# Optimization experiments

Measured on AMD Instinct MI355X. Metric: run time of the kernel, lower is better.

Reference implementation:

```python
import jax, jax.numpy as jnp
import numpy as np

START_IX = 62
END_IX = 63
NEG = -10000.0

def setup_inputs() -> dict:
    key = jax.random.key(0)
    k1, k2 = jax.random.split(key)
    B, S, T = 512, 1024, 64
    feats = jax.random.normal(k1, (B, S, T), dtype=jnp.float32)
    transitions = jax.random.normal(k2, (T, T), dtype=jnp.float32)
    # CRF constraints: nothing transitions into START; nothing transitions out of END
    transitions = transitions.at[START_IX, :].set(NEG).at[:, END_IX].set(NEG)
    return {"feats": feats, "transitions": transitions}

def reference(feats, transitions):
    # Viterbi decode (module forward). feats: [B,S,T], transitions: [T,T] (next, prev)
    B, S, T = feats.shape
    init = jnp.full((B, T), NEG, dtype=feats.dtype).at[:, START_IX].set(0.0)

    def step(fv, feat):  # fv [B,T], feat [B,T]
        # next_tag_var[b, next, prev] = fv[b, prev] + transitions[next, prev]
        nv = fv[:, None, :] + transitions[None, :, :]
        bp = jnp.argmax(nv, axis=2)                     # [B,T] best previous tag
        fv_new = jnp.max(nv, axis=2) + feat             # [B,T]
        return fv_new, bp

    fv, bptrs = jax.lax.scan(step, init, jnp.transpose(feats, (1, 0, 2)))  # bptrs [S,B,T]
    terminal = fv + transitions[END_IX][None, :]
    path_score = jnp.max(terminal, axis=1)              # [B]
    best_tag = jnp.argmax(terminal, axis=1)             # [B]

    def back(tag, bp):  # tag [B], bp [B,T]
        prev = jnp.take_along_axis(bp, tag[:, None], axis=1)[:, 0]
        return prev, tag

    _, tags_rev = jax.lax.scan(back, best_tag, bptrs[::-1])  # [S,B]: tags S-1..0
    best_path = jnp.transpose(tags_rev[::-1])                # [B,S]
    return path_score, best_path
```

## Files before the change

kernel.cpp:

```cpp
#include <hip/hip_runtime.h>

#define NEGV (-10000.0f)

constexpr int Bb = 512;
constexpr int Ss = 1024;
constexpr int Tt = 64;

typedef __attribute__((address_space(1))) const unsigned int guint_t;
typedef __attribute__((address_space(3))) unsigned int luint_t;

__global__ __launch_bounds__(256, 2) void viterbi_fused(
    const float* __restrict__ feats,
    const float* __restrict__ trans,
    float* __restrict__ path_score,
    float* __restrict__ best_path)
{
    __shared__ float ftile[2][8][Tt];
    __shared__ uint2 partials[2][4][Tt];
    __shared__ float fvb[4][16];
    __shared__ unsigned char bp_lds[Ss][Tt];
    __shared__ unsigned char ccomp[32][Tt];
    __shared__ int btags[32];

    const int b    = blockIdx.x;
    const int tid  = threadIdx.x;
    const int wid  = tid >> 6;
    const int lane = tid & 63;

    const float* fb = feats + (size_t)b * (Ss * Tt);

    const float* tr = trans + lane * Tt + (wid << 4);
    float4 t0 = *(const float4*)(tr + 0);
    float4 t1 = *(const float4*)(tr + 4);
    float4 t2 = *(const float4*)(tr + 8);
    float4 t3 = *(const float4*)(tr + 12);
    float tend = trans[63 * Tt + lane];

    if (wid == 0) {
#pragma unroll
        for (int i = 0; i < 2; ++i)
            __builtin_amdgcn_global_load_lds(
                (guint_t*)(fb + i * 256 + lane * 4),
                (luint_t*)((unsigned int*)&ftile[0][0][0] + i * 256),
                16, 0, 0);
        asm volatile("s_waitcnt vmcnt(0)" ::: "memory");
    }
    __syncthreads();

    float fv  = (lane == 62) ? 0.0f : NEGV;
    int  comp = lane;

    for (int t = 0; t < 128; ++t) {
        if (wid == 0 && t + 1 < 128) {
            const float* src = fb + (size_t)(t + 1) * 512;
            unsigned int* dst = (unsigned int*)&ftile[(t + 1) & 1][0][0];
#pragma unroll
            for (int i = 0; i < 2; ++i)
                __builtin_amdgcn_global_load_lds(
                    (guint_t*)(src + i * 256 + lane * 4),
                    (luint_t*)(dst + i * 256),
                    16, 0, 0);
        }
#pragma unroll
        for (int i = 0; i < 8; ++i) {
            const int s = t * 8 + i;
            float featv = ftile[t & 1][i][lane];

            if ((lane >> 4) == wid) fvb[wid][lane & 15] = fv;
            float4 q0 = *(float4*)&fvb[wid][0];
            float4 q1 = *(float4*)&fvb[wid][4];
            float4 q2 = *(float4*)&fvb[wid][8];
            float4 q3 = *(float4*)&fvb[wid][12];

            float mq0, mq1, mq2, mq3; int xq0, xq1, xq2, xq3;
#define QUAD(K, QV, TV, MQ, XQ) { \
            float ca = QV.x + TV.x, cb = QV.y + TV.y, cc = QV.z + TV.z, cd = QV.w + TV.w; \
            float mm = ca; int xx = 4*K + 0; \
            if (cb > mm) { mm = cb; xx = 4*K + 1; } \
            if (cc > mm) { mm = cc; xx = 4*K + 2; } \
            if (cd > mm) { mm = cd; xx = 4*K + 3; } \
            MQ = mm; XQ = xx; }
            QUAD(0, q0, t0, mq0, xq0)
            QUAD(1, q1, t1, mq1, xq1)
            QUAD(2, q2, t2, mq2, xq2)
            QUAD(3, q3, t3, mq3, xq3)
#undef QUAD
            float mp = mq0; int xp = xq0;
            if (mq1 > mp) { mp = mq1; xp = xq1; }
            if (mq2 > mp) { mp = mq2; xp = xq2; }
            if (mq3 > mp) { mp = mq3; xp = xq3; }
            int gix = (wid << 4) + xp;

            partials[i & 1][wid][lane] = make_uint2(__float_as_uint(mp), (unsigned)gix);

            if (i == 7) {
                asm volatile("" : "+v"(featv));
                if (wid == 0) asm volatile("s_waitcnt vmcnt(0)" ::: "memory");
            }
            __syncthreads();

            uint2 r0 = partials[i & 1][0][lane];
            uint2 r1 = partials[i & 1][1][lane];
            uint2 r2 = partials[i & 1][2][lane];
            uint2 r3 = partials[i & 1][3][lane];
            float mb = __uint_as_float(r0.x); int ib = (int)r0.y;
            float mw;
            mw = __uint_as_float(r1.x); if (mw > mb) { mb = mw; ib = (int)r1.y; }
            mw = __uint_as_float(r2.x); if (mw > mb) { mb = mw; ib = (int)r2.y; }
            mw = __uint_as_float(r3.x); if (mw > mb) { mb = mw; ib = (int)r3.y; }

            if (wid == 0) {
                bp_lds[s][lane] = (unsigned char)ib;
                comp = __shfl(comp, ib);
                if ((s & 31) == 31) { ccomp[s >> 5][lane] = (unsigned char)comp; comp = lane; }
            }
            fv = mb + featv;
        }
    }

    if (wid == 0) {
        float mr = fv + tend; int ir = lane;
#pragma unroll
        for (int off = 32; off >= 1; off >>= 1) {
            float mo = __shfl_xor(mr, off);
            int   io = __shfl_xor(ir, off);
            bool take = (mo > mr) || ((mo == mr) && (io < ir));
            mr = take ? mo : mr; ir = take ? io : ir;
        }
        if (lane == 0) {
            path_score[b] = mr;
            int tag = ir;
            for (int c = 31; c >= 0; --c) {
                btags[c] = tag;
                tag = ccomp[c][tag];
            }
        }
    }
    __syncthreads();

    if (wid == 0 && lane < 32) {
        int tag = btags[lane];
        float* op = best_path + (size_t)b * Ss + lane * 32;
        for (int i = 31; i >= 0; --i) {
            op[i] = (float)tag;
            tag = bp_lds[lane * 32 + i][tag];
        }
    }
}

extern "C" void kernel_launch(void* const* d_in, const int* in_sizes, int n_in,
                              void* d_out, int out_size, void* d_ws, size_t ws_size,
                              hipStream_t stream) {
    const float* feats = (const float*)d_in[0];
    const float* trans = (const float*)d_in[1];

    float* path_score = (float*)d_out;
    float* best_path  = (float*)d_out + Bb;

    viterbi_fused<<<Bb, 256, 0, stream>>>(feats, trans, path_score, best_path);
}
```

Before: 591.1 us.

## Broadcast fv via readlane and defer argmax byte resolution off the critical path

Replaces the LDS round-trip that broadcasts fv within each wave with v_readlane instructions, and moves argmax tracking out of the serial max chain. Only the max value is exchanged across waves before the barrier. Each wave then recovers its local index by equality match and writes one byte into a packed word. Wave 0 resolves the backpointer one step late, and the prefetch moves to wave 3 to lighten wave 0. This shortens the per-step critical path between barriers, at the cost of extra compare work, a deferred final step, and tie-breaking that now depends on exact float equality.

```diff
diff --git a/kernel.cpp b/kernel.cpp
--- a/kernel.cpp
+++ b/kernel.cpp
@@ -16,8 +16,8 @@
     float* __restrict__ best_path)
 {
     __shared__ float ftile[2][8][Tt];
-    __shared__ uint2 partials[2][4][Tt];
-    __shared__ float fvb[4][16];
+    __shared__ float vpart[2][4][Tt];
+    __shared__ unsigned int ipart[2][Tt];
     __shared__ unsigned char bp_lds[Ss][Tt];
     __shared__ unsigned char ccomp[32][Tt];
     __shared__ int btags[32];
@@ -26,17 +26,22 @@
     const int tid  = threadIdx.x;
     const int wid  = tid >> 6;
     const int lane = tid & 63;
+    const int base = wid << 4;
 
     const float* fb = feats + (size_t)b * (Ss * Tt);
 
-    const float* tr = trans + lane * Tt + (wid << 4);
-    float4 t0 = *(const float4*)(tr + 0);
-    float4 t1 = *(const float4*)(tr + 4);
-    float4 t2 = *(const float4*)(tr + 8);
-    float4 t3 = *(const float4*)(tr + 12);
+    float trow[16];
+    {
+        const float* tr = trans + lane * Tt + base;
+        float4* tv = (float4*)trow;
+        tv[0] = *(const float4*)(tr + 0);
+        tv[1] = *(const float4*)(tr + 4);
+        tv[2] = *(const float4*)(tr + 8);
+        tv[3] = *(const float4*)(tr + 12);
+    }
     float tend = trans[63 * Tt + lane];
 
-    if (wid == 0) {
+    if (wid == 3) {
 #pragma unroll
         for (int i = 0; i < 2; ++i)
             __builtin_amdgcn_global_load_lds(
@@ -51,7 +56,7 @@
     int  comp = lane;
 
     for (int t = 0; t < 128; ++t) {
-        if (wid == 0 && t + 1 < 128) {
+        if (wid == 3 && t + 1 < 128) {
             const float* src = fb + (size_t)(t + 1) * 512;
             unsigned int* dst = (unsigned int*)&ftile[(t + 1) & 1][0][0];
 #pragma unroll
@@ -64,61 +69,71 @@
 #pragma unroll
         for (int i = 0; i < 8; ++i) {
             const int s = t * 8 + i;
+            const int p = s & 1;
             float featv = ftile[t & 1][i][lane];
 
-            if ((lane >> 4) == wid) fvb[wid][lane & 15] = fv;
-            float4 q0 = *(float4*)&fvb[wid][0];
-            float4 q1 = *(float4*)&fvb[wid][4];
-            float4 q2 = *(float4*)&fvb[wid][8];
-            float4 q3 = *(float4*)&fvb[wid][12];
+            float c[16];
+#pragma unroll
+            for (int j = 0; j < 16; ++j) {
+                float g = __int_as_float(
+                    __builtin_amdgcn_readlane(__float_as_int(fv), base + j));
+                c[j] = g + trow[j];
+            }
+            float a0 = fmaxf(fmaxf(c[0],  c[1]),  c[2]);
+            float a1 = fmaxf(fmaxf(c[3],  c[4]),  c[5]);
+            float a2 = fmaxf(fmaxf(c[6],  c[7]),  c[8]);
+            float a3 = fmaxf(fmaxf(c[9],  c[10]), c[11]);
+            float a4 = fmaxf(fmaxf(c[12], c[13]), c[14]);
+            float m  = fmaxf(fmaxf(fmaxf(a0, a1), fmaxf(a2, a3)), fmaxf(a4, c[15]));
 
-            float mq0, mq1, mq2, mq3; int xq0, xq1, xq2, xq3;
-#define QUAD(K, QV, TV, MQ, XQ) { \
-            float ca = QV.x + TV.x, cb = QV.y + TV.y, cc = QV.z + TV.z, cd = QV.w + TV.w; \
-            float mm = ca; int xx = 4*K + 0; \
-            if (cb > mm) { mm = cb; xx = 4*K + 1; } \
-            if (cc > mm) { mm = cc; xx = 4*K + 2; } \
-            if (cd > mm) { mm = cd; xx = 4*K + 3; } \
-            MQ = mm; XQ = xx; }
-            QUAD(0, q0, t0, mq0, xq0)
-            QUAD(1, q1, t1, mq1, xq1)
-            QUAD(2, q2, t2, mq2, xq2)
-            QUAD(3, q3, t3, mq3, xq3)
-#undef QUAD
-            float mp = mq0; int xp = xq0;
-            if (mq1 > mp) { mp = mq1; xp = xq1; }
-            if (mq2 > mp) { mp = mq2; xp = xq2; }
-            if (mq3 > mp) { mp = mq3; xp = xq3; }
-            int gix = (wid << 4) + xp;
-
-            partials[i & 1][wid][lane] = make_uint2(__float_as_uint(mp), (unsigned)gix);
+            vpart[p][wid][lane] = m;
 
             if (i == 7) {
                 asm volatile("" : "+v"(featv));
-                if (wid == 0) asm volatile("s_waitcnt vmcnt(0)" ::: "memory");
+                if (wid == 3) asm volatile("s_waitcnt vmcnt(0)" ::: "memory");
             }
             __syncthreads();
 
-            uint2 r0 = partials[i & 1][0][lane];
-            uint2 r1 = partials[i & 1][1][lane];
-            uint2 r2 = partials[i & 1][2][lane];
-            uint2 r3 = partials[i & 1][3][lane];
-            float mb = __uint_as_float(r0.x); int ib = (int)r0.y;
-            float mw;
-            mw = __uint_as_float(r1.x); if (mw > mb) { mb = mw; ib = (int)r1.y; }
-            mw = __uint_as_float(r2.x); if (mw > mb) { mb = mw; ib = (int)r2.y; }
-            mw = __uint_as_float(r3.x); if (mw > mb) { mb = mw; ib = (int)r3.y; }
+            float v0 = vpart[p][0][lane];
+            float v1 = vpart[p][1][lane];
+            float v2 = vpart[p][2][lane];
+            float v3 = vpart[p][3][lane];
+            float mb = fmaxf(fmaxf(v0, v1), fmaxf(v2, v3));
 
-            if (wid == 0) {
-                bp_lds[s][lane] = (unsigned char)ib;
+            int jf = 15;
+#pragma unroll
+            for (int j = 14; j >= 0; --j) jf = (c[j] == mb) ? j : jf;
+            unsigned int byte = (m == mb) ? (unsigned)(base + jf) : 0xFFu;
+            ((unsigned char*)&ipart[p][0])[lane * 4 + wid] = (unsigned char)byte;
+
+            if (wid == 0 && s > 0) {
+                unsigned int u = ipart[1 - p][lane];
+                int b0 = u & 0xFF, b1 = (u >> 8) & 0xFF, b2 = (u >> 16) & 0xFF;
+                int b3 = u >> 24;
+                int ib = (b0 != 0xFF) ? b0 : (b1 != 0xFF) ? b1 : (b2 != 0xFF) ? b2 : b3;
+                bp_lds[s - 1][lane] = (unsigned char)ib;
                 comp = __shfl(comp, ib);
-                if ((s & 31) == 31) { ccomp[s >> 5][lane] = (unsigned char)comp; comp = lane; }
+                if (((s - 1) & 31) == 31) {
+                    ccomp[(s - 1) >> 5][lane] = (unsigned char)comp;
+                    comp = lane;
+                }
             }
             fv = mb + featv;
         }
     }
 
+    __syncthreads();
+
     if (wid == 0) {
+        {
+            unsigned int u = ipart[1][lane];
+            int b0 = u & 0xFF, b1 = (u >> 8) & 0xFF, b2 = (u >> 16) & 0xFF;
+            int b3 = u >> 24;
+            int ib = (b0 != 0xFF) ? b0 : (b1 != 0xFF) ? b1 : (b2 != 0xFF) ? b2 : b3;
+            bp_lds[1023][lane] = (unsigned char)ib;
+            comp = __shfl(comp, ib);
+            ccomp[31][lane] = (unsigned char)comp;
+        }
         float mr = fv + tend; int ir = lane;
 #pragma unroll
         for (int off = 32; off >= 1; off >>= 1) {
@@ -130,9 +145,9 @@
         if (lane == 0) {
             path_score[b] = mr;
             int tag = ir;
-            for (int c = 31; c >= 0; --c) {
-                btags[c] = tag;
-                tag = ccomp[c][tag];
+            for (int c2 = 31; c2 >= 0; --c2) {
+                btags[c2] = tag;
+                tag = ccomp[c2][tag];
             }
         }
     }
```

Measured after the change: 762.3 us. 1.29x slower.

## Run Viterbi forward pass in a single wave using DPP rotations

Applied to the files above, without the earlier changes.

Replaces the 4-wave block, which split the 64 previous tags across waves and merged partial argmaxes through shared memory with a barrier every step, with a single 64-lane wave per batch element. Each lane keeps its full transition row in registers, pre-permuted to match DPP row-rotate order, and walks over previous-tag scores with DPP rotations plus three cross-row shuffles. The winning index is then remapped back to a real tag. Feature rows are software-prefetched two steps ahead through plain global loads instead of async global-to-LDS copies. This removes per-step barriers and LDS traffic but leaves one wave per CU slot with 64 float registers of transitions, so each step is longer and serial and occupancy drops.

```diff
diff --git a/kernel.cpp b/kernel.cpp
--- a/kernel.cpp
+++ b/kernel.cpp
@@ -6,139 +6,123 @@
 constexpr int Ss = 1024;
 constexpr int Tt = 64;
 
-typedef __attribute__((address_space(1))) const unsigned int guint_t;
-typedef __attribute__((address_space(3))) unsigned int luint_t;
+__device__ __forceinline__ float dpp_ror1_f(float x) {
+    return __int_as_float(__builtin_amdgcn_update_dpp(
+        0, __float_as_int(x), 0x121, 0xF, 0xF, false));
+}
+__device__ __forceinline__ int dpp_ror1_i(int x) {
+    return __builtin_amdgcn_update_dpp(0, x, 0x121, 0xF, 0xF, false);
+}
 
-__global__ __launch_bounds__(256, 2) void viterbi_fused(
+__global__ __launch_bounds__(64, 1) void viterbi_wave(
     const float* __restrict__ feats,
     const float* __restrict__ trans,
     float* __restrict__ path_score,
     float* __restrict__ best_path)
 {
-    __shared__ float ftile[2][8][Tt];
-    __shared__ uint2 partials[2][4][Tt];
-    __shared__ float fvb[4][16];
     __shared__ unsigned char bp_lds[Ss][Tt];
     __shared__ unsigned char ccomp[32][Tt];
     __shared__ int btags[32];
 
     const int b    = blockIdx.x;
-    const int tid  = threadIdx.x;
-    const int wid  = tid >> 6;
-    const int lane = tid & 63;
-
+    const int lane = threadIdx.x;
     const float* fb = feats + (size_t)b * (Ss * Tt);
 
-    const float* tr = trans + lane * Tt + (wid << 4);
-    float4 t0 = *(const float4*)(tr + 0);
-    float4 t1 = *(const float4*)(tr + 4);
-    float4 t2 = *(const float4*)(tr + 8);
-    float4 t3 = *(const float4*)(tr + 12);
+    float* T_lds = (float*)&bp_lds[0][0];
+    {
+        float4*       dst = (float4*)T_lds;
+        const float4* src = (const float4*)trans;
+#pragma unroll
+        for (int i = 0; i < 16; ++i) dst[i * 64 + lane] = src[i * 64 + lane];
+    }
+    __syncthreads();
+
+    float trow[64];
+#pragma unroll
+    for (int r = 0; r < 4; ++r) {
+        int px = lane ^ (r << 4);
+#pragma unroll
+        for (int k = 0; k < 16; ++k) {
+            trow[r * 16 + k] = T_lds[lane * 64 + px];
+            px = dpp_ror1_i(px);
+        }
+    }
+    int d;
+    {
+        int p1 = dpp_ror1_i(lane);
+        d = (p1 - lane) & 15;
+    }
     float tend = trans[63 * Tt + lane];
-
-    if (wid == 0) {
-#pragma unroll
-        for (int i = 0; i < 2; ++i)
-            __builtin_amdgcn_global_load_lds(
-                (guint_t*)(fb + i * 256 + lane * 4),
-                (luint_t*)((unsigned int*)&ftile[0][0][0] + i * 256),
-                16, 0, 0);
-        asm volatile("s_waitcnt vmcnt(0)" ::: "memory");
-    }
     __syncthreads();
 
     float fv  = (lane == 62) ? 0.0f : NEGV;
     int  comp = lane;
+    float f0 = fb[lane];
+    float f1 = fb[Tt + lane];
 
-    for (int t = 0; t < 128; ++t) {
-        if (wid == 0 && t + 1 < 128) {
-            const float* src = fb + (size_t)(t + 1) * 512;
-            unsigned int* dst = (unsigned int*)&ftile[(t + 1) & 1][0][0];
-#pragma unroll
-            for (int i = 0; i < 2; ++i)
-                __builtin_amdgcn_global_load_lds(
-                    (guint_t*)(src + i * 256 + lane * 4),
-                    (luint_t*)(dst + i * 256),
-                    16, 0, 0);
-        }
-#pragma unroll
-        for (int i = 0; i < 8; ++i) {
-            const int s = t * 8 + i;
-            float featv = ftile[t & 1][i][lane];
-
-            if ((lane >> 4) == wid) fvb[wid][lane & 15] = fv;
-            float4 q0 = *(float4*)&fvb[wid][0];
-            float4 q1 = *(float4*)&fvb[wid][4];
-            float4 q2 = *(float4*)&fvb[wid][8];
-            float4 q3 = *(float4*)&fvb[wid][12];
-
-            float mq0, mq1, mq2, mq3; int xq0, xq1, xq2, xq3;
-#define QUAD(K, QV, TV, MQ, XQ) { \
-            float ca = QV.x + TV.x, cb = QV.y + TV.y, cc = QV.z + TV.z, cd = QV.w + TV.w; \
-            float mm = ca; int xx = 4*K + 0; \
-            if (cb > mm) { mm = cb; xx = 4*K + 1; } \
-            if (cc > mm) { mm = cc; xx = 4*K + 2; } \
-            if (cd > mm) { mm = cd; xx = 4*K + 3; } \
-            MQ = mm; XQ = xx; }
-            QUAD(0, q0, t0, mq0, xq0)
-            QUAD(1, q1, t1, mq1, xq1)
-            QUAD(2, q2, t2, mq2, xq2)
-            QUAD(3, q3, t3, mq3, xq3)
-#undef QUAD
-            float mp = mq0; int xp = xq0;
-            if (mq1 > mp) { mp = mq1; xp = xq1; }
-            if (mq2 > mp) { mp = mq2; xp = xq2; }
-            if (mq3 > mp) { mp = mq3; xp = xq3; }
-            int gix = (wid << 4) + xp;
-
-            partials[i & 1][wid][lane] = make_uint2(__float_as_uint(mp), (unsigned)gix);
-
-            if (i == 7) {
-                asm volatile("" : "+v"(featv));
-                if (wid == 0) asm volatile("s_waitcnt vmcnt(0)" ::: "memory");
-            }
-            __syncthreads();
-
-            uint2 r0 = partials[i & 1][0][lane];
-            uint2 r1 = partials[i & 1][1][lane];
-            uint2 r2 = partials[i & 1][2][lane];
-            uint2 r3 = partials[i & 1][3][lane];
-            float mb = __uint_as_float(r0.x); int ib = (int)r0.y;
-            float mw;
-            mw = __uint_as_float(r1.x); if (mw > mb) { mb = mw; ib = (int)r1.y; }
-            mw = __uint_as_float(r2.x); if (mw > mb) { mb = mw; ib = (int)r2.y; }
-            mw = __uint_as_float(r3.x); if (mw > mb) { mb = mw; ib = (int)r3.y; }
-
-            if (wid == 0) {
-                bp_lds[s][lane] = (unsigned char)ib;
-                comp = __shfl(comp, ib);
-                if ((s & 31) == 31) { ccomp[s >> 5][lane] = (unsigned char)comp; comp = lane; }
-            }
-            fv = mb + featv;
-        }
+#define PHASE(R, XR, MR, KR)                                        \
+    {                                                               \
+        float xr = XR;                                              \
+        MR = xr + trow[(R) * 16];                                   \
+        KR = (R) * 16;                                              \
+        _Pragma("unroll")                                           \
+        for (int k = (R) * 16 + 1; k < (R) * 16 + 16; ++k) {        \
+            xr = dpp_ror1_f(xr);                                    \
+            float c = xr + trow[k];                                 \
+            if (c > MR) { MR = c; KR = k; }                         \
+        }                                                           \
     }
 
-    if (wid == 0) {
-        float mr = fv + tend; int ir = lane;
+    for (int s = 0; s < Ss; ++s) {
+        int sp = s + 2; sp = sp < Ss ? sp : Ss - 1;
+        float f2 = fb[(size_t)sp * Tt + lane];
+
+        float x0 = fv;
+        float x1 = __shfl(fv, lane ^ 16);
+        float x2 = __shfl(fv, lane ^ 32);
+        float x3 = __shfl(fv, lane ^ 48);
+
+        float m0, m1, m2, m3; int k0, k1, k2, k3;
+        PHASE(0, x0, m0, k0)
+        PHASE(1, x1, m1, k1)
+        PHASE(2, x2, m2, k2)
+        PHASE(3, x3, m3, k3)
+
+        float m = m0; int kk = k0;
+        if (m1 > m) { m = m1; kk = k1; }
+        if (m2 > m) { m = m2; kk = k2; }
+        if (m3 > m) { m = m3; kk = k3; }
+
+        int p = ((lane + d * (kk & 15)) & 15) | ((lane ^ kk) & 48);
+
+        bp_lds[s][lane] = (unsigned char)p;
+        comp = __shfl(comp, p);
+        if ((s & 31) == 31) { ccomp[s >> 5][lane] = (unsigned char)comp; comp = lane; }
+
+        fv = m + f0;
+        f0 = f1; f1 = f2;
+    }
+#undef PHASE
+
+    float mr = fv + tend; int ir = lane;
 #pragma unroll
-        for (int off = 32; off >= 1; off >>= 1) {
-            float mo = __shfl_xor(mr, off);
-            int   io = __shfl_xor(ir, off);
-            bool take = (mo > mr) || ((mo == mr) && (io < ir));
-            mr = take ? mo : mr; ir = take ? io : ir;
-        }
-        if (lane == 0) {
-            path_score[b] = mr;
-            int tag = ir;
-            for (int c = 31; c >= 0; --c) {
-                btags[c] = tag;
-                tag = ccomp[c][tag];
-            }
+    for (int off = 32; off >= 1; off >>= 1) {
+        float mo = __shfl_xor(mr, off);
+        int   io = __shfl_xor(ir, off);
+        bool take = (mo > mr) || ((mo == mr) && (io < ir));
+        mr = take ? mo : mr; ir = take ? io : ir;
+    }
+    if (lane == 0) {
+        path_score[b] = mr;
+        int tag = ir;
+        for (int c2 = 31; c2 >= 0; --c2) {
+            btags[c2] = tag;
+            tag = ccomp[c2][tag];
         }
     }
     __syncthreads();
 
-    if (wid == 0 && lane < 32) {
+    if (lane < 32) {
         int tag = btags[lane];
         float* op = best_path + (size_t)b * Ss + lane * 32;
         for (int i = 31; i >= 0; --i) {
@@ -157,5 +141,5 @@
     float* path_score = (float*)d_out;
     float* best_path  = (float*)d_out + Bb;
 
-    viterbi_fused<<<Bb, 256, 0, stream>>>(feats, trans, path_score, best_path);
+    viterbi_wave<<<Bb, 64, 0, stream>>>(feats, trans, path_score, best_path);
 }
```

After: 1.069 ms. 1.81x slower.
